# Kernel optimization log

Hardware: AMD Instinct MI355X
Metric: run time of the kernel (lower is better)

Reference implementation:

```python
import jax, jax.numpy as jnp
import numpy as np

T, B, D = 200, 2048, 256
H1, H2, H3 = 512, 256, 1
LABEL_LEN = 10


def _linear_init(key, fan_in, fan_out):
    lim = 1.0 / np.sqrt(fan_in)
    kw, kb = jax.random.split(key)
    W = jax.random.uniform(kw, (fan_in, fan_out), minval=-lim, maxval=lim, dtype=jnp.float32)
    b = jax.random.uniform(kb, (fan_out,), minval=-lim, maxval=lim, dtype=jnp.float32)
    return W, b


def setup_inputs() -> dict:
    key = jax.random.key(0)
    ks = jax.random.split(key, 8)
    inputs = jax.random.normal(ks[0], (T, B, D), dtype=jnp.float32)  # padded, time-major [T,B,D]
    lengths = jnp.sort(jax.random.randint(ks[1], (B,), LABEL_LEN, T + 1))[::-1]
    lengths = lengths.at[0].set(T)  # packed-seq: descending lengths, max = T
    ctr_W1, ctr_b1 = _linear_init(ks[2], D, H1)
    ctr_W2, ctr_b2 = _linear_init(ks[3], H1, H2)
    ctr_W3, ctr_b3 = _linear_init(ks[4], H2, H3)
    cvr_W1, cvr_b1 = _linear_init(ks[5], D, H1)
    cvr_W2, cvr_b2 = _linear_init(ks[6], H1, H2)
    cvr_W3, cvr_b3 = _linear_init(ks[7], H2, H3)
    return dict(inputs=inputs, lengths=lengths, label_len=LABEL_LEN,
                ctr_W1=ctr_W1, ctr_b1=ctr_b1, ctr_W2=ctr_W2, ctr_b2=ctr_b2,
                ctr_W3=ctr_W3, ctr_b3=ctr_b3,
                cvr_W1=cvr_W1, cvr_b1=cvr_b1, cvr_W2=cvr_W2, cvr_b2=cvr_b2,
                cvr_W3=cvr_W3, cvr_b3=cvr_b3)


def _tower(x, W1, b1, W2, b2, W3, b3):
    # Dropout is identity in eval; LeakyReLU slope 0.01 (torch default).
    x = jax.nn.leaky_relu(x @ W1 + b1)
    x = jax.nn.leaky_relu(x @ W2 + b2)
    x = jax.nn.leaky_relu(x @ W3 + b3)
    return x


def reference(inputs, lengths, label_len,
              ctr_W1, ctr_b1, ctr_W2, ctr_b2, ctr_W3, ctr_b3,
              cvr_W1, cvr_b1, cvr_W2, cvr_b2, cvr_W3, cvr_b3):
    # f1: O(T) prefix-sum replaces the original O(T^2) per-step torch.mean loop.
    cs = jnp.cumsum(inputs, axis=0)                              # [T,B,D]
    # h[j,k] = mean over prefix of length L_j - label_len + k + 1
    idx = lengths[:, None] - label_len + jnp.arange(label_len)   # [B,label_len], time index
    cs_bt = cs.transpose(1, 0, 2)                                # [B,T,D]
    h = jnp.take_along_axis(cs_bt, idx[:, :, None], axis=1)      # [B,label_len,D]
    h = h / (idx[:, :, None] + 1).astype(inputs.dtype)
    h_ctr = jax.nn.sigmoid(_tower(h, ctr_W1, ctr_b1, ctr_W2, ctr_b2, ctr_W3, ctr_b3))
    h_cvr = jax.nn.sigmoid(_tower(h, cvr_W1, cvr_b1, cvr_W2, cvr_b2, cvr_W3, cvr_b3))
    return h_ctr * h_cvr                                         # [B,label_len,1]
```

## Files before the change

kernel.cpp:

```cpp
#include <hip/hip_runtime.h>
#include <math.h>

#define B_DIM 2048
#define D_DIM 256
#define H1 512
#define H2 256
#define LBL 10
#define M_ROWS (B_DIM * LBL)
#define LD_A1 520
#define WSZ1 (H1 * D_DIM)
#define WSZ2 (H2 * H1)

typedef __attribute__((ext_vector_type(8))) short frag_ab;
typedef __attribute__((ext_vector_type(4))) float frag_cd;

__device__ __forceinline__ float leaky(float v) { return v > 0.f ? v : 0.01f * v; }

__device__ __forceinline__ unsigned short f2bf(float f) {
  union { float f; unsigned int u; } v;
  v.f = f;
  unsigned int r = v.u + 0x7FFFu + ((v.u >> 16) & 1u);
  return (unsigned short)(r >> 16);
}

__device__ __forceinline__ void acc4(float4& s, const float4 a) {
  s.x += a.x; s.y += a.y; s.z += a.z; s.w += a.w;
}

__global__ __launch_bounds__(256) void prefix_kernel(
    const float* __restrict__ x, const int* __restrict__ lens,
    unsigned short* __restrict__ hb) {
  const int wv = threadIdx.x >> 6;
  const int lane = threadIdx.x & 63;
  const int b = blockIdx.x * 4 + wv;
  const int L = lens[b];
  const int Lm = L - LBL;
  const size_t ts = (size_t)(B_DIM * D_DIM / 4);
  const float4* xb = reinterpret_cast<const float4*>(x) + (size_t)b * (D_DIM / 4) + lane;
  float4 s0 = make_float4(0.f, 0.f, 0.f, 0.f), s1 = s0, s2 = s0, s3 = s0;
  int t = 0;
  for (; t + 8 <= Lm; t += 8) {
    float4 a0 = xb[(size_t)(t + 0) * ts], a1 = xb[(size_t)(t + 1) * ts];
    float4 a2 = xb[(size_t)(t + 2) * ts], a3 = xb[(size_t)(t + 3) * ts];
    float4 a4 = xb[(size_t)(t + 4) * ts], a5 = xb[(size_t)(t + 5) * ts];
    float4 a6 = xb[(size_t)(t + 6) * ts], a7 = xb[(size_t)(t + 7) * ts];
    acc4(s0, a0); acc4(s1, a1); acc4(s2, a2); acc4(s3, a3);
    acc4(s0, a4); acc4(s1, a5); acc4(s2, a6); acc4(s3, a7);
  }
  for (; t < Lm; ++t) acc4(s0, xb[(size_t)t * ts]);
  acc4(s0, s1); acc4(s2, s3); acc4(s0, s2);
  #pragma unroll
  for (int k = 0; k < LBL; ++k) {
    const int tt = Lm + k;
    acc4(s0, xb[(size_t)tt * ts]);
    const float inv = 1.0f / (float)(tt + 1);
    ushort4 o;
    o.x = f2bf(s0.x * inv); o.y = f2bf(s0.y * inv);
    o.z = f2bf(s0.z * inv); o.w = f2bf(s0.w * inv);
    *reinterpret_cast<ushort4*>(hb + (size_t)(b * LBL + k) * D_DIM + lane * 4) = o;
  }
}

__global__ __launch_bounds__(256) void pack1_kernel(
    const float* __restrict__ Wa, const float* __restrict__ Wb,
    unsigned short* __restrict__ P1) {
  const int idx = blockIdx.x * 256 + threadIdx.x;
  const int tw = blockIdx.y;
  const float* __restrict__ in = tw ? Wb : Wa;
  const int l = idx & 63;
  const int n = (idx >> 6) & 15;
  const int ks = (idx >> 10) & 7;
  const int cbh = idx >> 13;
  const int col = cbh * 256 + n * 16 + (l & 15);
  const int k0 = ks * 32 + (l >> 4) * 8;
  unsigned short o[8];
  #pragma unroll
  for (int jj = 0; jj < 8; ++jj)
    o[jj] = f2bf(in[(size_t)(k0 + jj) * H1 + col]);
  ushort4* dst = reinterpret_cast<ushort4*>(P1 + (size_t)tw * WSZ1 + (size_t)idx * 8);
  dst[0] = make_ushort4(o[0], o[1], o[2], o[3]);
  dst[1] = make_ushort4(o[4], o[5], o[6], o[7]);
}

__global__ __launch_bounds__(256) void pack2_kernel(
    const float* __restrict__ Wa, const float* __restrict__ Wb,
    unsigned short* __restrict__ P2) {
  const int idx = blockIdx.x * 256 + threadIdx.x;
  const int tw = blockIdx.y;
  const float* __restrict__ in = tw ? Wb : Wa;
  const int l = idx & 63;
  const int n = (idx >> 6) & 7;
  const int ks = (idx >> 9) & 15;
  const int cbh = idx >> 13;
  const int col = cbh * 128 + n * 16 + (l & 15);
  const int k0 = ks * 32 + (l >> 4) * 8;
  unsigned short o[8];
  #pragma unroll
  for (int jj = 0; jj < 8; ++jj)
    o[jj] = f2bf(in[(size_t)(k0 + jj) * H2 + col]);
  ushort4* dst = reinterpret_cast<ushort4*>(P2 + (size_t)tw * WSZ2 + (size_t)idx * 8);
  dst[0] = make_ushort4(o[0], o[1], o[2], o[3]);
  dst[1] = make_ushort4(o[4], o[5], o[6], o[7]);
}

__global__ __launch_bounds__(256, 4) void tower_mfma(
    const unsigned short* __restrict__ hb,
    const unsigned short* __restrict__ P1,
    const unsigned short* __restrict__ P2,
    const float* __restrict__ b1a, const float* __restrict__ b2a,
    const float* __restrict__ w3a, const float* __restrict__ b3a,
    const float* __restrict__ b1b, const float* __restrict__ b2b,
    const float* __restrict__ w3b, const float* __restrict__ b3b,
    float* __restrict__ sigbuf) {
  __shared__ unsigned short A1[32][LD_A1];
  __shared__ float part[2][32];
  const int tid = threadIdx.x;
  const int l = tid & 63;
  const int w = tid >> 6;
  const int lr = l & 15;
  const int lg = l >> 4;
  const int rb = (w & 1) * 16;
  const int cbh = w >> 1;
  const int r0 = blockIdx.x * 32;
  const int tw = blockIdx.y;

  const unsigned short* __restrict__ pb1 =
      P1 + (size_t)tw * WSZ1 + (size_t)cbh * (WSZ1 / 2) + (size_t)l * 8;
  const unsigned short* __restrict__ pb2 =
      P2 + (size_t)tw * WSZ2 + (size_t)cbh * (WSZ2 / 2) + (size_t)l * 8;
  const float* __restrict__ B1 = tw ? b1b : b1a;
  const float* __restrict__ B2 = tw ? b2b : b2a;
  const float* __restrict__ W3 = tw ? w3b : w3a;
  const float* __restrict__ B3 = tw ? b3b : b3a;

  frag_cd acc1[16];
  #pragma unroll
  for (int n = 0; n < 16; ++n) {
    const float bv = B1[cbh * 256 + n * 16 + lr];
    acc1[n] = (frag_cd){bv, bv, bv, bv};
  }
  const unsigned short* arow = hb + (size_t)(r0 + rb + lr) * D_DIM;
  #pragma unroll
  for (int ks = 0; ks < D_DIM / 32; ++ks) {
    const frag_ab af = *reinterpret_cast<const frag_ab*>(arow + ks * 32 + lg * 8);
    #pragma unroll
    for (int n = 0; n < 16; ++n) {
      const frag_ab bf =
          *reinterpret_cast<const frag_ab*>(pb1 + (size_t)(ks * 16 + n) * 512);
      acc1[n] = __builtin_amdgcn_mfma_f32_16x16x32_bf16(af, bf, acc1[n], 0, 0, 0);
    }
  }
  #pragma unroll
  for (int n = 0; n < 16; ++n)
    #pragma unroll
    for (int r = 0; r < 4; ++r)
      A1[rb + lg * 4 + r][cbh * 256 + n * 16 + lr] = f2bf(leaky(acc1[n][r]));
  __syncthreads();

  frag_cd acc2[8];
  #pragma unroll
  for (int n = 0; n < 8; ++n) {
    const float bv = B2[cbh * 128 + n * 16 + lr];
    acc2[n] = (frag_cd){bv, bv, bv, bv};
  }
  #pragma unroll
  for (int ks = 0; ks < H1 / 32; ++ks) {
    const frag_ab af = *reinterpret_cast<const frag_ab*>(&A1[rb + lr][ks * 32 + lg * 8]);
    #pragma unroll
    for (int n = 0; n < 8; ++n) {
      const frag_ab bf =
          *reinterpret_cast<const frag_ab*>(pb2 + (size_t)(ks * 8 + n) * 512);
      acc2[n] = __builtin_amdgcn_mfma_f32_16x16x32_bf16(af, bf, acc2[n], 0, 0, 0);
    }
  }

  float s[4] = {0.f, 0.f, 0.f, 0.f};
  #pragma unroll
  for (int n = 0; n < 8; ++n) {
    const float w3v = W3[cbh * 128 + n * 16 + lr];
    #pragma unroll
    for (int r = 0; r < 4; ++r)
      s[r] = fmaf(leaky(acc2[n][r]), w3v, s[r]);
  }
  #pragma unroll
  for (int r = 0; r < 4; ++r) {
    s[r] += __shfl_xor(s[r], 1);
    s[r] += __shfl_xor(s[r], 2);
    s[r] += __shfl_xor(s[r], 4);
    s[r] += __shfl_xor(s[r], 8);
  }
  if (lr == 0) {
    #pragma unroll
    for (int r = 0; r < 4; ++r) part[cbh][rb + lg * 4 + r] = s[r];
  }
  __syncthreads();
  if (tid < 32) {
    const float z = leaky(part[0][tid] + part[1][tid] + B3[0]);
    sigbuf[(size_t)tw * M_ROWS + r0 + tid] = 1.f / (1.f + expf(-z));
  }
}

__global__ __launch_bounds__(256) void combine_kernel(
    const float* __restrict__ sigbuf, float* __restrict__ out) {
  const int i = blockIdx.x * 256 + threadIdx.x;
  out[i] = sigbuf[i] * sigbuf[M_ROWS + i];
}

extern "C" void kernel_launch(void* const* d_in, const int* in_sizes, int n_in,
                              void* d_out, int out_size, void* d_ws, size_t ws_size,
                              hipStream_t stream) {
  (void)in_sizes; (void)n_in; (void)out_size; (void)ws_size;
  const float* x    = (const float*)d_in[0];
  const int*   lens = (const int*)d_in[1];
  const float* cW1 = (const float*)d_in[3];
  const float* cb1 = (const float*)d_in[4];
  const float* cW2 = (const float*)d_in[5];
  const float* cb2 = (const float*)d_in[6];
  const float* cW3 = (const float*)d_in[7];
  const float* cb3 = (const float*)d_in[8];
  const float* vW1 = (const float*)d_in[9];
  const float* vb1 = (const float*)d_in[10];
  const float* vW2 = (const float*)d_in[11];
  const float* vb2 = (const float*)d_in[12];
  const float* vW3 = (const float*)d_in[13];
  const float* vb3 = (const float*)d_in[14];
  float* out = (float*)d_out;

  unsigned short* hb = (unsigned short*)d_ws;
  unsigned short* p1 = hb + (size_t)M_ROWS * D_DIM;
  unsigned short* p2 = p1 + 2 * WSZ1;
  float* sigbuf = (float*)(p2 + 2 * WSZ2);

  prefix_kernel<<<B_DIM / 4, 256, 0, stream>>>(x, lens, hb);
  pack1_kernel<<<dim3(WSZ1 / 8 / 256, 2), 256, 0, stream>>>(cW1, vW1, p1);
  pack2_kernel<<<dim3(WSZ2 / 8 / 256, 2), 256, 0, stream>>>(cW2, vW2, p2);

  tower_mfma<<<dim3(M_ROWS / 32, 2), 256, 0, stream>>>(
      hb, p1, p2, cb1, cb2, cW3, cb3, vb1, vb2, vW3, vb3, sigbuf);
  combine_kernel<<<M_ROWS / 256, 256, 0, stream>>>(sigbuf, out);
}
```

Measured before the change: 99.39 us.

## Double row tile in tower MFMA kernel and interleave prefix batch order

The tower kernel now processes 64 rows per block instead of 32, so each wave computes two 16-row MFMA tiles and reuses each weight fragment loaded from global memory across both. This halves weight traffic per row but doubles accumulator registers, so launch bounds drop to two blocks per SM. The prefix kernel also interleaves long and short sequences (index i alternates between b and B-1-b) so each block gets balanced work, since lengths are sorted descending.

```diff
diff --git a/kernel.cpp b/kernel.cpp
--- a/kernel.cpp
+++ b/kernel.cpp
@@ -32,7 +32,8 @@
     unsigned short* __restrict__ hb) {
   const int wv = threadIdx.x >> 6;
   const int lane = threadIdx.x & 63;
-  const int b = blockIdx.x * 4 + wv;
+  const int idx = blockIdx.x * 4 + wv;
+  const int b = (idx & 1) ? (B_DIM - 1 - (idx >> 1)) : (idx >> 1);
   const int L = lens[b];
   const int Lm = L - LBL;
   const size_t ts = (size_t)(B_DIM * D_DIM / 4);
@@ -103,7 +104,7 @@
   dst[1] = make_ushort4(o[4], o[5], o[6], o[7]);
 }
 
-__global__ __launch_bounds__(256, 4) void tower_mfma(
+__global__ __launch_bounds__(256, 2) void tower_mfma(
     const unsigned short* __restrict__ hb,
     const unsigned short* __restrict__ P1,
     const unsigned short* __restrict__ P2,
@@ -112,16 +113,16 @@
     const float* __restrict__ b1b, const float* __restrict__ b2b,
     const float* __restrict__ w3b, const float* __restrict__ b3b,
     float* __restrict__ sigbuf) {
-  __shared__ unsigned short A1[32][LD_A1];
-  __shared__ float part[2][32];
+  __shared__ unsigned short A1[64][LD_A1];
+  __shared__ float part[2][64];
   const int tid = threadIdx.x;
   const int l = tid & 63;
   const int w = tid >> 6;
   const int lr = l & 15;
   const int lg = l >> 4;
-  const int rb = (w & 1) * 16;
+  const int rb = (w & 1) * 32;
   const int cbh = w >> 1;
-  const int r0 = blockIdx.x * 32;
+  const int r0 = blockIdx.x * 64;
   const int tw = blockIdx.y;
 
   const unsigned short* __restrict__ pb1 =
@@ -133,68 +134,87 @@
   const float* __restrict__ W3 = tw ? w3b : w3a;
   const float* __restrict__ B3 = tw ? b3b : b3a;
 
-  frag_cd acc1[16];
+  frag_cd acc1[2][16];
   #pragma unroll
   for (int n = 0; n < 16; ++n) {
     const float bv = B1[cbh * 256 + n * 16 + lr];
-    acc1[n] = (frag_cd){bv, bv, bv, bv};
-  }
-  const unsigned short* arow = hb + (size_t)(r0 + rb + lr) * D_DIM;
+    acc1[0][n] = (frag_cd){bv, bv, bv, bv};
+    acc1[1][n] = (frag_cd){bv, bv, bv, bv};
+  }
+  const unsigned short* arow0 = hb + (size_t)(r0 + rb + lr) * D_DIM;
+  const unsigned short* arow1 = hb + (size_t)(r0 + rb + 16 + lr) * D_DIM;
   #pragma unroll
   for (int ks = 0; ks < D_DIM / 32; ++ks) {
-    const frag_ab af = *reinterpret_cast<const frag_ab*>(arow + ks * 32 + lg * 8);
+    const frag_ab af0 = *reinterpret_cast<const frag_ab*>(arow0 + ks * 32 + lg * 8);
+    const frag_ab af1 = *reinterpret_cast<const frag_ab*>(arow1 + ks * 32 + lg * 8);
     #pragma unroll
     for (int n = 0; n < 16; ++n) {
       const frag_ab bf =
           *reinterpret_cast<const frag_ab*>(pb1 + (size_t)(ks * 16 + n) * 512);
-      acc1[n] = __builtin_amdgcn_mfma_f32_16x16x32_bf16(af, bf, acc1[n], 0, 0, 0);
+      acc1[0][n] = __builtin_amdgcn_mfma_f32_16x16x32_bf16(af0, bf, acc1[0][n], 0, 0, 0);
+      acc1[1][n] = __builtin_amdgcn_mfma_f32_16x16x32_bf16(af1, bf, acc1[1][n], 0, 0, 0);
     }
   }
   #pragma unroll
-  for (int n = 0; n < 16; ++n)
-    #pragma unroll
-    for (int r = 0; r < 4; ++r)
-      A1[rb + lg * 4 + r][cbh * 256 + n * 16 + lr] = f2bf(leaky(acc1[n][r]));
+  for (int m = 0; m < 2; ++m)
+    #pragma unroll
+    for (int n = 0; n < 16; ++n)
+      #pragma unroll
+      for (int r = 0; r < 4; ++r)
+        A1[rb + m * 16 + lg * 4 + r][cbh * 256 + n * 16 + lr] =
+            f2bf(leaky(acc1[m][n][r]));
   __syncthreads();
 
-  frag_cd acc2[8];
+  frag_cd acc2[2][8];
   #pragma unroll
   for (int n = 0; n < 8; ++n) {
     const float bv = B2[cbh * 128 + n * 16 + lr];
-    acc2[n] = (frag_cd){bv, bv, bv, bv};
+    acc2[0][n] = (frag_cd){bv, bv, bv, bv};
+    acc2[1][n] = (frag_cd){bv, bv, bv, bv};
   }
   #pragma unroll
   for (int ks = 0; ks < H1 / 32; ++ks) {
-    const frag_ab af = *reinterpret_cast<const frag_ab*>(&A1[rb + lr][ks * 32 + lg * 8]);
+    const frag_ab af0 =
+        *reinterpret_cast<const frag_ab*>(&A1[rb + lr][ks * 32 + lg * 8]);
+    const frag_ab af1 =
+        *reinterpret_cast<const frag_ab*>(&A1[rb + 16 + lr][ks * 32 + lg * 8]);
     #pragma unroll
     for (int n = 0; n < 8; ++n) {
       const frag_ab bf =
           *reinterpret_cast<const frag_ab*>(pb2 + (size_t)(ks * 8 + n) * 512);
-      acc2[n] = __builtin_amdgcn_mfma_f32_16x16x32_bf16(af, bf, acc2[n], 0, 0, 0);
+      acc2[0][n] = __builtin_amdgcn_mfma_f32_16x16x32_bf16(af0, bf, acc2[0][n], 0, 0, 0);
+      acc2[1][n] = __builtin_amdgcn_mfma_f32_16x16x32_bf16(af1, bf, acc2[1][n], 0, 0, 0);
     }
   }
 
-  float s[4] = {0.f, 0.f, 0.f, 0.f};
+  float s[2][4] = {{0.f, 0.f, 0.f, 0.f}, {0.f, 0.f, 0.f, 0.f}};
   #pragma unroll
   for (int n = 0; n < 8; ++n) {
     const float w3v = W3[cbh * 128 + n * 16 + lr];
     #pragma unroll
-    for (int r = 0; r < 4; ++r)
-      s[r] = fmaf(leaky(acc2[n][r]), w3v, s[r]);
-  }
-  #pragma unroll
-  for (int r = 0; r < 4; ++r) {
-    s[r] += __shfl_xor(s[r], 1);
-    s[r] += __shfl_xor(s[r], 2);
-    s[r] += __shfl_xor(s[r], 4);
-    s[r] += __shfl_xor(s[r], 8);
-  }
+    for (int m = 0; m < 2; ++m)
+      #pragma unroll
+      for (int r = 0; r < 4; ++r)
+        s[m][r] = fmaf(leaky(acc2[m][n][r]), w3v, s[m][r]);
+  }
+  #pragma unroll
+  for (int m = 0; m < 2; ++m)
+    #pragma unroll
+    for (int r = 0; r < 4; ++r) {
+      s[m][r] += __shfl_xor(s[m][r], 1);
+      s[m][r] += __shfl_xor(s[m][r], 2);
+      s[m][r] += __shfl_xor(s[m][r], 4);
+      s[m][r] += __shfl_xor(s[m][r], 8);
+    }
   if (lr == 0) {
     #pragma unroll
-    for (int r = 0; r < 4; ++r) part[cbh][rb + lg * 4 + r] = s[r];
+    for (int m = 0; m < 2; ++m)
+      #pragma unroll
+      for (int r = 0; r < 4; ++r)
+        part[cbh][rb + m * 16 + lg * 4 + r] = s[m][r];
   }
   __syncthreads();
-  if (tid < 32) {
+  if (tid < 64) {
     const float z = leaky(part[0][tid] + part[1][tid] + B3[0]);
     sigbuf[(size_t)tw * M_ROWS + r0 + tid] = 1.f / (1.f + expf(-z));
   }
@@ -235,7 +255,7 @@
   pack1_kernel<<<dim3(WSZ1 / 8 / 256, 2), 256, 0, stream>>>(cW1, vW1, p1);
   pack2_kernel<<<dim3(WSZ2 / 8 / 256, 2), 256, 0, stream>>>(cW2, vW2, p2);
 
-  tower_mfma<<<dim3(M_ROWS / 32, 2), 256, 0, stream>>>(
+  tower_mfma<<<dim3(M_ROWS / 64, 2), 256, 0, stream>>>(
       hb, p1, p2, cb1, cb2, cW3, cb3, vb1, vb2, vW3, vb3, sigbuf);
   combine_kernel<<<M_ROWS / 256, 256, 0, stream>>>(sigbuf, out);
 }
```

Result: slower. 107.0 us (+7.6%).

## Switch tower GEMMs to 32x32x16 MFMA with four column-split waves

Applied to the files above, without the earlier changes.

Switches the tower kernel's matrix instructions from 16x16x32 to 32x32x16 bf16 MFMA. Each wave now covers all 32 rows and a quarter of the output columns instead of 16 rows and half the columns. The weight packing layout is changed to match, and the two pack kernels are merged into one launch. The goal is fewer MFMA issues and fewer B-fragment loads per output, plus one less launch. In exchange the final reduction needs more shuffle steps and the occupancy hint in the launch bounds is dropped.

```diff
diff --git a/kernel.cpp b/kernel.cpp
--- a/kernel.cpp
+++ b/kernel.cpp
@@ -12,7 +12,7 @@
 #define WSZ2 (H2 * H1)
 
 typedef __attribute__((ext_vector_type(8))) short frag_ab;
-typedef __attribute__((ext_vector_type(4))) float frag_cd;
+typedef __attribute__((ext_vector_type(16))) float f32x16;
 
 __device__ __forceinline__ float leaky(float v) { return v > 0.f ? v : 0.01f * v; }
 
@@ -61,49 +61,46 @@
   }
 }
 
-__global__ __launch_bounds__(256) void pack1_kernel(
-    const float* __restrict__ Wa, const float* __restrict__ Wb,
-    unsigned short* __restrict__ P1) {
-  const int idx = blockIdx.x * 256 + threadIdx.x;
+__global__ __launch_bounds__(256) void pack_kernel(
+    const float* __restrict__ W1a, const float* __restrict__ W1b,
+    const float* __restrict__ W2a, const float* __restrict__ W2b,
+    unsigned short* __restrict__ P1, unsigned short* __restrict__ P2) {
   const int tw = blockIdx.y;
-  const float* __restrict__ in = tw ? Wb : Wa;
-  const int l = idx & 63;
-  const int n = (idx >> 6) & 15;
-  const int ks = (idx >> 10) & 7;
-  const int cbh = idx >> 13;
-  const int col = cbh * 256 + n * 16 + (l & 15);
-  const int k0 = ks * 32 + (l >> 4) * 8;
-  unsigned short o[8];
-  #pragma unroll
-  for (int jj = 0; jj < 8; ++jj)
-    o[jj] = f2bf(in[(size_t)(k0 + jj) * H1 + col]);
-  ushort4* dst = reinterpret_cast<ushort4*>(P1 + (size_t)tw * WSZ1 + (size_t)idx * 8);
-  dst[0] = make_ushort4(o[0], o[1], o[2], o[3]);
-  dst[1] = make_ushort4(o[4], o[5], o[6], o[7]);
-}
-
-__global__ __launch_bounds__(256) void pack2_kernel(
-    const float* __restrict__ Wa, const float* __restrict__ Wb,
-    unsigned short* __restrict__ P2) {
-  const int idx = blockIdx.x * 256 + threadIdx.x;
-  const int tw = blockIdx.y;
-  const float* __restrict__ in = tw ? Wb : Wa;
-  const int l = idx & 63;
-  const int n = (idx >> 6) & 7;
-  const int ks = (idx >> 9) & 15;
-  const int cbh = idx >> 13;
-  const int col = cbh * 128 + n * 16 + (l & 15);
-  const int k0 = ks * 32 + (l >> 4) * 8;
-  unsigned short o[8];
-  #pragma unroll
-  for (int jj = 0; jj < 8; ++jj)
-    o[jj] = f2bf(in[(size_t)(k0 + jj) * H2 + col]);
-  ushort4* dst = reinterpret_cast<ushort4*>(P2 + (size_t)tw * WSZ2 + (size_t)idx * 8);
-  dst[0] = make_ushort4(o[0], o[1], o[2], o[3]);
-  dst[1] = make_ushort4(o[4], o[5], o[6], o[7]);
-}
-
-__global__ __launch_bounds__(256, 4) void tower_mfma(
+  const int bx = blockIdx.x;
+  if (bx < 64) {
+    const int idx = bx * 256 + threadIdx.x;
+    const float* __restrict__ in = tw ? W1b : W1a;
+    const int l = idx & 63;
+    const int nt = (idx >> 6) & 3;
+    const int ks = (idx >> 8) & 15;
+    const int w = idx >> 12;
+    const int col = w * 128 + nt * 32 + (l & 31);
+    const int k0 = ks * 16 + (l >> 5) * 8;
+    unsigned short o[8];
+    #pragma unroll
+    for (int j = 0; j < 8; ++j) o[j] = f2bf(in[(size_t)(k0 + j) * H1 + col]);
+    ushort4* dst = reinterpret_cast<ushort4*>(P1 + (size_t)tw * WSZ1 + (size_t)idx * 8);
+    dst[0] = make_ushort4(o[0], o[1], o[2], o[3]);
+    dst[1] = make_ushort4(o[4], o[5], o[6], o[7]);
+  } else {
+    const int idx = (bx - 64) * 256 + threadIdx.x;
+    const float* __restrict__ in = tw ? W2b : W2a;
+    const int l = idx & 63;
+    const int nt = (idx >> 6) & 1;
+    const int ks = (idx >> 7) & 31;
+    const int w = idx >> 12;
+    const int col = w * 64 + nt * 32 + (l & 31);
+    const int k0 = ks * 16 + (l >> 5) * 8;
+    unsigned short o[8];
+    #pragma unroll
+    for (int j = 0; j < 8; ++j) o[j] = f2bf(in[(size_t)(k0 + j) * H2 + col]);
+    ushort4* dst = reinterpret_cast<ushort4*>(P2 + (size_t)tw * WSZ2 + (size_t)idx * 8);
+    dst[0] = make_ushort4(o[0], o[1], o[2], o[3]);
+    dst[1] = make_ushort4(o[4], o[5], o[6], o[7]);
+  }
+}
+
+__global__ __launch_bounds__(256) void tower_mfma(
     const unsigned short* __restrict__ hb,
     const unsigned short* __restrict__ P1,
     const unsigned short* __restrict__ P2,
@@ -113,89 +110,97 @@
     const float* __restrict__ w3b, const float* __restrict__ b3b,
     float* __restrict__ sigbuf) {
   __shared__ unsigned short A1[32][LD_A1];
-  __shared__ float part[2][32];
+  __shared__ float part[4][32];
   const int tid = threadIdx.x;
   const int l = tid & 63;
   const int w = tid >> 6;
-  const int lr = l & 15;
-  const int lg = l >> 4;
-  const int rb = (w & 1) * 16;
-  const int cbh = w >> 1;
+  const int lc = l & 31;
+  const int hi = l >> 5;
   const int r0 = blockIdx.x * 32;
   const int tw = blockIdx.y;
 
   const unsigned short* __restrict__ pb1 =
-      P1 + (size_t)tw * WSZ1 + (size_t)cbh * (WSZ1 / 2) + (size_t)l * 8;
+      P1 + (size_t)tw * WSZ1 + (size_t)w * (WSZ1 / 4) + (size_t)l * 8;
   const unsigned short* __restrict__ pb2 =
-      P2 + (size_t)tw * WSZ2 + (size_t)cbh * (WSZ2 / 2) + (size_t)l * 8;
+      P2 + (size_t)tw * WSZ2 + (size_t)w * (WSZ2 / 4) + (size_t)l * 8;
   const float* __restrict__ B1 = tw ? b1b : b1a;
   const float* __restrict__ B2 = tw ? b2b : b2a;
   const float* __restrict__ W3 = tw ? w3b : w3a;
   const float* __restrict__ B3 = tw ? b3b : b3a;
 
-  frag_cd acc1[16];
-  #pragma unroll
-  for (int n = 0; n < 16; ++n) {
-    const float bv = B1[cbh * 256 + n * 16 + lr];
-    acc1[n] = (frag_cd){bv, bv, bv, bv};
-  }
-  const unsigned short* arow = hb + (size_t)(r0 + rb + lr) * D_DIM;
-  #pragma unroll
-  for (int ks = 0; ks < D_DIM / 32; ++ks) {
-    const frag_ab af = *reinterpret_cast<const frag_ab*>(arow + ks * 32 + lg * 8);
-    #pragma unroll
-    for (int n = 0; n < 16; ++n) {
+  f32x16 acc1[4];
+  #pragma unroll
+  for (int nt = 0; nt < 4; ++nt) {
+    const float bv = B1[w * 128 + nt * 32 + lc];
+    #pragma unroll
+    for (int r = 0; r < 16; ++r) acc1[nt][r] = bv;
+  }
+  const unsigned short* arow = hb + (size_t)(r0 + lc) * D_DIM + hi * 8;
+  #pragma unroll
+  for (int ks = 0; ks < D_DIM / 16; ++ks) {
+    const frag_ab af = *reinterpret_cast<const frag_ab*>(arow + ks * 16);
+    #pragma unroll
+    for (int nt = 0; nt < 4; ++nt) {
       const frag_ab bf =
-          *reinterpret_cast<const frag_ab*>(pb1 + (size_t)(ks * 16 + n) * 512);
-      acc1[n] = __builtin_amdgcn_mfma_f32_16x16x32_bf16(af, bf, acc1[n], 0, 0, 0);
+          *reinterpret_cast<const frag_ab*>(pb1 + (size_t)(ks * 4 + nt) * 512);
+      acc1[nt] = __builtin_amdgcn_mfma_f32_32x32x16_bf16(af, bf, acc1[nt], 0, 0, 0);
     }
   }
   #pragma unroll
-  for (int n = 0; n < 16; ++n)
-    #pragma unroll
-    for (int r = 0; r < 4; ++r)
-      A1[rb + lg * 4 + r][cbh * 256 + n * 16 + lr] = f2bf(leaky(acc1[n][r]));
+  for (int nt = 0; nt < 4; ++nt)
+    #pragma unroll
+    for (int r = 0; r < 16; ++r) {
+      const int row = (r & 3) + 8 * (r >> 2) + 4 * hi;
+      A1[row][w * 128 + nt * 32 + lc] = f2bf(leaky(acc1[nt][r]));
+    }
   __syncthreads();
 
-  frag_cd acc2[8];
-  #pragma unroll
-  for (int n = 0; n < 8; ++n) {
-    const float bv = B2[cbh * 128 + n * 16 + lr];
-    acc2[n] = (frag_cd){bv, bv, bv, bv};
-  }
-  #pragma unroll
-  for (int ks = 0; ks < H1 / 32; ++ks) {
-    const frag_ab af = *reinterpret_cast<const frag_ab*>(&A1[rb + lr][ks * 32 + lg * 8]);
-    #pragma unroll
-    for (int n = 0; n < 8; ++n) {
+  f32x16 acc2[2];
+  #pragma unroll
+  for (int nt = 0; nt < 2; ++nt) {
+    const float bv = B2[w * 64 + nt * 32 + lc];
+    #pragma unroll
+    for (int r = 0; r < 16; ++r) acc2[nt][r] = bv;
+  }
+  #pragma unroll
+  for (int ks = 0; ks < H1 / 16; ++ks) {
+    const frag_ab af =
+        *reinterpret_cast<const frag_ab*>(&A1[lc][ks * 16 + hi * 8]);
+    #pragma unroll
+    for (int nt = 0; nt < 2; ++nt) {
       const frag_ab bf =
-          *reinterpret_cast<const frag_ab*>(pb2 + (size_t)(ks * 8 + n) * 512);
-      acc2[n] = __builtin_amdgcn_mfma_f32_16x16x32_bf16(af, bf, acc2[n], 0, 0, 0);
+          *reinterpret_cast<const frag_ab*>(pb2 + (size_t)(ks * 2 + nt) * 512);
+      acc2[nt] = __builtin_amdgcn_mfma_f32_32x32x16_bf16(af, bf, acc2[nt], 0, 0, 0);
     }
   }
 
-  float s[4] = {0.f, 0.f, 0.f, 0.f};
-  #pragma unroll
-  for (int n = 0; n < 8; ++n) {
-    const float w3v = W3[cbh * 128 + n * 16 + lr];
-    #pragma unroll
-    for (int r = 0; r < 4; ++r)
-      s[r] = fmaf(leaky(acc2[n][r]), w3v, s[r]);
-  }
-  #pragma unroll
-  for (int r = 0; r < 4; ++r) {
-    s[r] += __shfl_xor(s[r], 1);
-    s[r] += __shfl_xor(s[r], 2);
-    s[r] += __shfl_xor(s[r], 4);
-    s[r] += __shfl_xor(s[r], 8);
-  }
-  if (lr == 0) {
-    #pragma unroll
-    for (int r = 0; r < 4; ++r) part[cbh][rb + lg * 4 + r] = s[r];
+  float rsum[16];
+  #pragma unroll
+  for (int r = 0; r < 16; ++r) rsum[r] = 0.f;
+  #pragma unroll
+  for (int nt = 0; nt < 2; ++nt) {
+    const float w3v = W3[w * 64 + nt * 32 + lc];
+    #pragma unroll
+    for (int r = 0; r < 16; ++r)
+      rsum[r] = fmaf(leaky(acc2[nt][r]), w3v, rsum[r]);
+  }
+  #pragma unroll
+  for (int r = 0; r < 16; ++r) {
+    rsum[r] += __shfl_xor(rsum[r], 1);
+    rsum[r] += __shfl_xor(rsum[r], 2);
+    rsum[r] += __shfl_xor(rsum[r], 4);
+    rsum[r] += __shfl_xor(rsum[r], 8);
+    rsum[r] += __shfl_xor(rsum[r], 16);
+  }
+  if (lc == 0) {
+    #pragma unroll
+    for (int r = 0; r < 16; ++r)
+      part[w][(r & 3) + 8 * (r >> 2) + 4 * hi] = rsum[r];
   }
   __syncthreads();
   if (tid < 32) {
-    const float z = leaky(part[0][tid] + part[1][tid] + B3[0]);
+    const float z =
+        leaky(part[0][tid] + part[1][tid] + part[2][tid] + part[3][tid] + B3[0]);
     sigbuf[(size_t)tw * M_ROWS + r0 + tid] = 1.f / (1.f + expf(-z));
   }
 }
@@ -232,9 +237,7 @@
   float* sigbuf = (float*)(p2 + 2 * WSZ2);
 
   prefix_kernel<<<B_DIM / 4, 256, 0, stream>>>(x, lens, hb);
-  pack1_kernel<<<dim3(WSZ1 / 8 / 256, 2), 256, 0, stream>>>(cW1, vW1, p1);
-  pack2_kernel<<<dim3(WSZ2 / 8 / 256, 2), 256, 0, stream>>>(cW2, vW2, p2);
-
+  pack_kernel<<<dim3(128, 2), 256, 0, stream>>>(cW1, vW1, cW2, vW2, p1, p2);
   tower_mfma<<<dim3(M_ROWS / 32, 2), 256, 0, stream>>>(
       hb, p1, p2, cb1, cb2, cW3, cb3, vb1, vb2, vW3, vb3, sigbuf);
   combine_kernel<<<M_ROWS / 256, 256, 0, stream>>>(sigbuf, out);
```

Result: slower. 110.0 us (+10.6%).

## Fuse prefix and weight-pack kernels; split each sequence's time sum across four waves

Applied to the files above, without the earlier changes.

Merges the prefix-sum kernel and both weight-packing kernels into one prologue launch, with block ranges picking the role. The prefix work now gives each batch row a whole block, splitting its time range across four waves and reducing through shared memory, instead of one wave per row. Blocks alternate between long and short sequences to even out the load. This is meant to cut launch overhead and raise memory-level parallelism on the bandwidth-bound prefix sum, at the cost of a block-level sync and three idle waves during the final label-step tail.

```diff
diff --git a/kernel.cpp b/kernel.cpp
--- a/kernel.cpp
+++ b/kernel.cpp
@@ -27,19 +27,69 @@
   s.x += a.x; s.y += a.y; s.z += a.z; s.w += a.w;
 }
 
-__global__ __launch_bounds__(256) void prefix_kernel(
+__global__ __launch_bounds__(256) void prologue_kernel(
     const float* __restrict__ x, const int* __restrict__ lens,
-    unsigned short* __restrict__ hb) {
-  const int wv = threadIdx.x >> 6;
-  const int lane = threadIdx.x & 63;
-  const int b = blockIdx.x * 4 + wv;
+    unsigned short* __restrict__ hb,
+    const float* __restrict__ W1a, const float* __restrict__ W1b,
+    const float* __restrict__ W2a, const float* __restrict__ W2b,
+    unsigned short* __restrict__ P1, unsigned short* __restrict__ P2) {
+  __shared__ float4 partial[4][64];
+  const int bx = blockIdx.x;
+  const int tid = threadIdx.x;
+
+  if (bx < 128) {
+    const int tw = bx >> 6;
+    const int idx = (bx & 63) * 256 + tid;
+    const float* __restrict__ in = tw ? W1b : W1a;
+    const int l = idx & 63;
+    const int n = (idx >> 6) & 15;
+    const int ks = (idx >> 10) & 7;
+    const int cbh = idx >> 13;
+    const int col = cbh * 256 + n * 16 + (l & 15);
+    const int k0 = ks * 32 + (l >> 4) * 8;
+    unsigned short o[8];
+    #pragma unroll
+    for (int jj = 0; jj < 8; ++jj)
+      o[jj] = f2bf(in[(size_t)(k0 + jj) * H1 + col]);
+    ushort4* dst = reinterpret_cast<ushort4*>(P1 + (size_t)tw * WSZ1 + (size_t)idx * 8);
+    dst[0] = make_ushort4(o[0], o[1], o[2], o[3]);
+    dst[1] = make_ushort4(o[4], o[5], o[6], o[7]);
+    return;
+  }
+  if (bx < 256) {
+    const int pb = bx - 128;
+    const int tw = pb >> 6;
+    const int idx = (pb & 63) * 256 + tid;
+    const float* __restrict__ in = tw ? W2b : W2a;
+    const int l = idx & 63;
+    const int n = (idx >> 6) & 7;
+    const int ks = (idx >> 9) & 15;
+    const int cbh = idx >> 13;
+    const int col = cbh * 128 + n * 16 + (l & 15);
+    const int k0 = ks * 32 + (l >> 4) * 8;
+    unsigned short o[8];
+    #pragma unroll
+    for (int jj = 0; jj < 8; ++jj)
+      o[jj] = f2bf(in[(size_t)(k0 + jj) * H2 + col]);
+    ushort4* dst = reinterpret_cast<ushort4*>(P2 + (size_t)tw * WSZ2 + (size_t)idx * 8);
+    dst[0] = make_ushort4(o[0], o[1], o[2], o[3]);
+    dst[1] = make_ushort4(o[4], o[5], o[6], o[7]);
+    return;
+  }
+
+  const int wv = tid >> 6;
+  const int lane = tid & 63;
+  const int bid = bx - 256;
+  const int b = (bid & 1) ? (B_DIM - 1 - (bid >> 1)) : (bid >> 1);
   const int L = lens[b];
   const int Lm = L - LBL;
   const size_t ts = (size_t)(B_DIM * D_DIM / 4);
   const float4* xb = reinterpret_cast<const float4*>(x) + (size_t)b * (D_DIM / 4) + lane;
+  const int c0 = (Lm * wv) >> 2;
+  const int c1 = (wv == 3) ? Lm : ((Lm * (wv + 1)) >> 2);
   float4 s0 = make_float4(0.f, 0.f, 0.f, 0.f), s1 = s0, s2 = s0, s3 = s0;
-  int t = 0;
-  for (; t + 8 <= Lm; t += 8) {
+  int t = c0;
+  for (; t + 8 <= c1; t += 8) {
     float4 a0 = xb[(size_t)(t + 0) * ts], a1 = xb[(size_t)(t + 1) * ts];
     float4 a2 = xb[(size_t)(t + 2) * ts], a3 = xb[(size_t)(t + 3) * ts];
     float4 a4 = xb[(size_t)(t + 4) * ts], a5 = xb[(size_t)(t + 5) * ts];
@@ -47,60 +97,26 @@
     acc4(s0, a0); acc4(s1, a1); acc4(s2, a2); acc4(s3, a3);
     acc4(s0, a4); acc4(s1, a5); acc4(s2, a6); acc4(s3, a7);
   }
-  for (; t < Lm; ++t) acc4(s0, xb[(size_t)t * ts]);
+  for (; t < c1; ++t) acc4(s0, xb[(size_t)t * ts]);
   acc4(s0, s1); acc4(s2, s3); acc4(s0, s2);
-  #pragma unroll
-  for (int k = 0; k < LBL; ++k) {
-    const int tt = Lm + k;
-    acc4(s0, xb[(size_t)tt * ts]);
-    const float inv = 1.0f / (float)(tt + 1);
-    ushort4 o;
-    o.x = f2bf(s0.x * inv); o.y = f2bf(s0.y * inv);
-    o.z = f2bf(s0.z * inv); o.w = f2bf(s0.w * inv);
-    *reinterpret_cast<ushort4*>(hb + (size_t)(b * LBL + k) * D_DIM + lane * 4) = o;
-  }
-}
-
-__global__ __launch_bounds__(256) void pack1_kernel(
-    const float* __restrict__ Wa, const float* __restrict__ Wb,
-    unsigned short* __restrict__ P1) {
-  const int idx = blockIdx.x * 256 + threadIdx.x;
-  const int tw = blockIdx.y;
-  const float* __restrict__ in = tw ? Wb : Wa;
-  const int l = idx & 63;
-  const int n = (idx >> 6) & 15;
-  const int ks = (idx >> 10) & 7;
-  const int cbh = idx >> 13;
-  const int col = cbh * 256 + n * 16 + (l & 15);
-  const int k0 = ks * 32 + (l >> 4) * 8;
-  unsigned short o[8];
-  #pragma unroll
-  for (int jj = 0; jj < 8; ++jj)
-    o[jj] = f2bf(in[(size_t)(k0 + jj) * H1 + col]);
-  ushort4* dst = reinterpret_cast<ushort4*>(P1 + (size_t)tw * WSZ1 + (size_t)idx * 8);
-  dst[0] = make_ushort4(o[0], o[1], o[2], o[3]);
-  dst[1] = make_ushort4(o[4], o[5], o[6], o[7]);
-}
-
-__global__ __launch_bounds__(256) void pack2_kernel(
-    const float* __restrict__ Wa, const float* __restrict__ Wb,
-    unsigned short* __restrict__ P2) {
-  const int idx = blockIdx.x * 256 + threadIdx.x;
-  const int tw = blockIdx.y;
-  const float* __restrict__ in = tw ? Wb : Wa;
-  const int l = idx & 63;
-  const int n = (idx >> 6) & 7;
-  const int ks = (idx >> 9) & 15;
-  const int cbh = idx >> 13;
-  const int col = cbh * 128 + n * 16 + (l & 15);
-  const int k0 = ks * 32 + (l >> 4) * 8;
-  unsigned short o[8];
-  #pragma unroll
-  for (int jj = 0; jj < 8; ++jj)
-    o[jj] = f2bf(in[(size_t)(k0 + jj) * H2 + col]);
-  ushort4* dst = reinterpret_cast<ushort4*>(P2 + (size_t)tw * WSZ2 + (size_t)idx * 8);
-  dst[0] = make_ushort4(o[0], o[1], o[2], o[3]);
-  dst[1] = make_ushort4(o[4], o[5], o[6], o[7]);
+  partial[wv][lane] = s0;
+  __syncthreads();
+  if (wv == 3) {
+    float4 s = partial[0][lane];
+    acc4(s, partial[1][lane]);
+    acc4(s, partial[2][lane]);
+    acc4(s, partial[3][lane]);
+    #pragma unroll
+    for (int k = 0; k < LBL; ++k) {
+      const int tt = Lm + k;
+      acc4(s, xb[(size_t)tt * ts]);
+      const float inv = 1.0f / (float)(tt + 1);
+      ushort4 o;
+      o.x = f2bf(s.x * inv); o.y = f2bf(s.y * inv);
+      o.z = f2bf(s.z * inv); o.w = f2bf(s.w * inv);
+      *reinterpret_cast<ushort4*>(hb + (size_t)(b * LBL + k) * D_DIM + lane * 4) = o;
+    }
+  }
 }
 
 __global__ __launch_bounds__(256, 4) void tower_mfma(
@@ -231,10 +247,8 @@
   unsigned short* p2 = p1 + 2 * WSZ1;
   float* sigbuf = (float*)(p2 + 2 * WSZ2);
 
-  prefix_kernel<<<B_DIM / 4, 256, 0, stream>>>(x, lens, hb);
-  pack1_kernel<<<dim3(WSZ1 / 8 / 256, 2), 256, 0, stream>>>(cW1, vW1, p1);
-  pack2_kernel<<<dim3(WSZ2 / 8 / 256, 2), 256, 0, stream>>>(cW2, vW2, p2);
-
+  prologue_kernel<<<256 + B_DIM, 256, 0, stream>>>(
+      x, lens, hb, cW1, vW1, cW2, vW2, p1, p2);
   tower_mfma<<<dim3(M_ROWS / 32, 2), 256, 0, stream>>>(
       hb, p1, p2, cb1, cb2, cW3, cb3, vb1, vb2, vW3, vb3, sigbuf);
   combine_kernel<<<M_ROWS / 256, 256, 0, stream>>>(sigbuf, out);
```

Measured after the change: 101.7 us. 1.02x slower.
